# Kernel tuning notes

Measured on AMD Instinct MI355X. Metric: run time of the kernel, lower is better.

Reference implementation:

```python
import jax, jax.numpy as jnp
import numpy as np

B, T, C, V = 8, 2048, 256, 1024


def setup_inputs() -> dict:
    key = jax.random.key(0)
    k1, k2 = jax.random.split(key)
    z = jax.random.normal(k1, (B, T, C), dtype=jnp.float32)
    codebook = jax.random.normal(k2, (V, C), dtype=jnp.float32)
    mask = jnp.ones((B, T, 1), dtype=jnp.float32)
    return {"z": z, "codebook": codebook, "mask": mask}


def reference(z, codebook, mask):
    # e = codebook.embedding.weight.clone().detach()
    e = jax.lax.stop_gradient(codebook)            # (V, C)
    b, t, c = z.shape
    v = e.shape[0]
    zf = z.reshape(-1, c)                          # (B*T, C)
    # squared distances: ||z||^2 + ||e||^2 - 2 z e^T
    d = (jnp.sum(zf * zf, axis=1, keepdims=True)
         + jnp.sum(e * e, axis=1)
         - 2.0 * zf @ e.T)                         # (B*T, V)
    idx = jnp.argmin(d, axis=1)                    # (B*T,)
    # one-hot scatter + matmul gather == direct gather
    z_q = e[idx].reshape(b, t, c)
    z_q = z_q * mask
    pad_e = e[0]                                   # (C,)
    z_q = jnp.where(mask == 0, pad_e, z_q)
    # masked MSE commitment loss
    valid_count = jnp.sum(mask) * c
    commitment_loss = jnp.sum((z - jax.lax.stop_gradient(z_q)) ** 2 * mask) / valid_count
    # straight-through estimator
    z_q = z + jax.lax.stop_gradient(z_q - z)
    min_encoding_indices = idx.reshape(b, t)
    # run-length dedup (deterministic: keep first element of each run),
    # compacted to the front and padded with pad_e to static length T
    keep = jnp.concatenate(
        [jnp.ones((b, 1), bool),
         min_encoding_indices[:, 1:] != min_encoding_indices[:, :-1]], axis=1)
    order = jnp.argsort(jnp.where(keep, 0, 1), axis=1, stable=True)  # kept positions first
    gathered = jnp.take_along_axis(z_q, order[:, :, None], axis=1)
    kept_sorted = jnp.take_along_axis(keep, order, axis=1)
    z_q_disc = jnp.where(kept_sorted[:, :, None], gathered, pad_e)
    # softmax diversity loss over soft assignments
    soft = jax.nn.softmax(-d, axis=1)              # (B*T, V)
    hist = jnp.sum(soft * mask.reshape(-1, 1), axis=0)  # (V,)
    p = hist / (jnp.sum(hist) + 1e-8)
    diversity_loss = jnp.sum(p * jnp.log(p * v + 1e-8))
    return (commitment_loss, diversity_loss, z_q, z_q_disc, min_encoding_indices)
```

## Files before the change

kernel.cpp:

```cpp
#include <hip/hip_runtime.h>
#include <math.h>

#define NB 8
#define NT 2048
#define NC 256
#define NV 1024
#define BT (NB*NT)

typedef __attribute__((ext_vector_type(8)))  short bf16x8;
typedef __attribute__((ext_vector_type(8)))  short short8v;
typedef __attribute__((ext_vector_type(16))) float f32x16;

#define HIST_OFF  0
#define EN_OFF    4096
#define CPART_OFF 8192
#define ORD_OFF   16384
#define KC_OFF    77824
#define WS_REQ    77856

__device__ __forceinline__ float bf_hi(float v, short* bits) {
  unsigned u = __float_as_uint(v);
  *bits = (short)(u >> 16);
  return __uint_as_float(u & 0xffff0000u);
}

__global__ __launch_bounds__(256) void vq_prep_e(
    const float* __restrict__ e, short* __restrict__ e1,
    short* __restrict__ e2, short* __restrict__ e3)
{
  __shared__ float el[32 * NC];
  const int t = threadIdx.x, cb = blockIdx.x;
  {
    const int r = t >> 3, cc = (t & 7) * 32;
    const float* er = e + (size_t)(cb * 32 + r) * NC + cc;
    float* dst = el + r * NC + cc;
    #pragma unroll
    for (int i = 0; i < 8; ++i) *(float4*)(dst + i * 4) = *(const float4*)(er + i * 4);
  }
  __syncthreads();
  const int s = t >> 4, h = (t >> 3) & 1, rb = (t & 7) * 4;
  const int kb = s * 16 + h * 8;
  #pragma unroll
  for (int rr = 0; rr < 4; ++rr) {
    short8v p1, p2, p3;
    #pragma unroll
    for (int ii = 0; ii < 8; ++ii) {
      float v = el[(rb + rr) * NC + kb + ii];
      short b1, b2, b3;
      float f1 = bf_hi(v, &b1);
      float r1 = v - f1;
      float f2 = bf_hi(r1, &b2);
      float r2 = r1 - f2;
      bf_hi(r2, &b3);
      p1[ii] = b1; p2[ii] = b2; p3[ii] = b3;
    }
    size_t off = (size_t)(s * 2 + h) * 8192 + (size_t)(cb * 32 + rb + rr) * 8;
    *(short8v*)(e1 + off) = p1;
    *(short8v*)(e2 + off) = p2;
    *(short8v*)(e3 + off) = p3;
  }
}

__global__ void vq_enorm(const float* __restrict__ e, float* __restrict__ en) {
  int c = blockIdx.x, t = threadIdx.x;
  float v = e[(size_t)c * NC + t];
  float s = v * v;
  #pragma unroll
  for (int off = 32; off; off >>= 1) s += __shfl_down(s, off, 64);
  __shared__ float w4[4];
  if ((t & 63) == 0) w4[t >> 6] = s;
  __syncthreads();
  if (t == 0) en[c] = w4[0] + w4[1] + w4[2] + w4[3];
}

__global__ __launch_bounds__(512, 4) void vq_main_fused(
    const float* __restrict__ z,
    const short* __restrict__ eT1, const short* __restrict__ eT2, const short* __restrict__ eT3,
    const float* __restrict__ en, const float* __restrict__ mask,
    float* __restrict__ hist, float* __restrict__ idxf)
{
  __shared__ short zl1[8192], zl2[8192], zl3[8192];
  __shared__ float pmv[32][8];
  __shared__ int   pmi[32][8];
  __shared__ float psum[32][8];
  __shared__ float mfin[32];
  __shared__ float wrow[32];

  const int tid  = threadIdx.x;
  const int lane = tid & 63, wv = tid >> 6;
  const int l31  = lane & 31, half = lane >> 5;
  const int b = blockIdx.x, row0 = b * 32;

  {
    const int s = tid >> 5, r = tid & 31;
    const float* zp = z + (size_t)(row0 + r) * NC + s * 16;
    float v[16];
    #pragma unroll
    for (int i = 0; i < 4; ++i) *(float4*)(v + i * 4) = *(const float4*)(zp + i * 4);
    #pragma unroll
    for (int hh = 0; hh < 2; ++hh) {
      short8v p1, p2, p3;
      #pragma unroll
      for (int ii = 0; ii < 8; ++ii) {
        float x = v[hh * 8 + ii];
        short b1, b2, b3;
        float f1 = bf_hi(x, &b1);
        float r1 = x - f1;
        float f2 = bf_hi(r1, &b2);
        float r2 = r1 - f2;
        bf_hi(r2, &b3);
        p1[ii] = b1; p2[ii] = b2; p3[ii] = b3;
      }
      const int off = s * 512 + hh * 256 + r * 8;
      *(short8v*)&zl1[off] = p1;
      *(short8v*)&zl2[off] = p2;
      *(short8v*)&zl3[off] = p3;
    }
  }
  __syncthreads();

  f32x16 acc[4];
  #pragma unroll
  for (int t = 0; t < 4; ++t)
    #pragma unroll
    for (int r = 0; r < 16; ++r) acc[t][r] = 0.f;

  for (int s = 0; s < 16; ++s) {
    const int aoff = s * 512 + half * 256 + l31 * 8;
    const bf16x8 a1 = *(const bf16x8*)&zl1[aoff];
    const bf16x8 a2 = *(const bf16x8*)&zl2[aoff];
    const bf16x8 a3 = *(const bf16x8*)&zl3[aoff];
    const size_t bbase = (size_t)(s * 2 + half) * 8192 + (size_t)(wv * 128 + l31) * 8;
    #pragma unroll
    for (int t = 0; t < 4; ++t) {
      const size_t bo = bbase + (size_t)(t * 32) * 8;
      const bf16x8 b1 = *(const bf16x8*)(eT1 + bo);
      const bf16x8 b2 = *(const bf16x8*)(eT2 + bo);
      const bf16x8 b3 = *(const bf16x8*)(eT3 + bo);
      acc[t] = __builtin_amdgcn_mfma_f32_32x32x16_bf16(a1, b1, acc[t], 0, 0, 0);
      acc[t] = __builtin_amdgcn_mfma_f32_32x32x16_bf16(a2, b1, acc[t], 0, 0, 0);
      acc[t] = __builtin_amdgcn_mfma_f32_32x32x16_bf16(a3, b1, acc[t], 0, 0, 0);
      acc[t] = __builtin_amdgcn_mfma_f32_32x32x16_bf16(a1, b2, acc[t], 0, 0, 0);
      acc[t] = __builtin_amdgcn_mfma_f32_32x32x16_bf16(a2, b2, acc[t], 0, 0, 0);
      acc[t] = __builtin_amdgcn_mfma_f32_32x32x16_bf16(a1, b3, acc[t], 0, 0, 0);
    }
  }

  float enr[4];
  #pragma unroll
  for (int t = 0; t < 4; ++t) enr[t] = en[wv * 128 + t * 32 + l31];
  #pragma unroll
  for (int t = 0; t < 4; ++t)
    #pragma unroll
    for (int r = 0; r < 16; ++r) acc[t][r] = fmaf(-2.f, acc[t][r], enr[t]);

  float bv[16]; int bi[16];
  #pragma unroll
  for (int r = 0; r < 16; ++r) {
    bv[r] = acc[0][r]; bi[r] = wv * 128 + l31;
    #pragma unroll
    for (int t = 1; t < 4; ++t) {
      float vv = acc[t][r]; int cc = wv * 128 + t * 32 + l31;
      if (vv < bv[r]) { bv[r] = vv; bi[r] = cc; }
    }
    #pragma unroll
    for (int off = 1; off <= 16; off <<= 1) {
      float ov = __shfl_xor(bv[r], off, 64);
      int   oi = __shfl_xor(bi[r], off, 64);
      if (ov < bv[r] || (ov == bv[r] && oi < bi[r])) { bv[r] = ov; bi[r] = oi; }
    }
  }
  if (l31 == 0) {
    #pragma unroll
    for (int r = 0; r < 16; ++r) {
      int row = (r & 3) + 8 * (r >> 2) + 4 * half;
      pmv[row][wv] = bv[r]; pmi[row][wv] = bi[r];
    }
  }
  __syncthreads();
  if (tid < 32) {
    float mv = pmv[tid][0]; int mi = pmi[tid][0];
    #pragma unroll
    for (int w = 1; w < 8; ++w) {
      float v = pmv[tid][w]; int i2 = pmi[tid][w];
      if (v < mv || (v == mv && i2 < mi)) { mv = v; mi = i2; }
    }
    mfin[tid] = mv;
    idxf[row0 + tid] = (float)mi;
  }
  __syncthreads();

  #pragma unroll
  for (int r = 0; r < 16; ++r) {
    float m = mfin[(r & 3) + 8 * (r >> 2) + 4 * half];
    float s0 = 0.f;
    #pragma unroll
    for (int t = 0; t < 4; ++t) {
      float p = __expf(m - acc[t][r]);
      acc[t][r] = p; s0 += p;
    }
    #pragma unroll
    for (int off = 1; off <= 16; off <<= 1) s0 += __shfl_xor(s0, off, 64);
    if (l31 == 0) psum[(r & 3) + 8 * (r >> 2) + 4 * half][wv] = s0;
  }
  __syncthreads();
  if (tid < 32) {
    float s0 = 0.f;
    #pragma unroll
    for (int w = 0; w < 8; ++w) s0 += psum[tid][w];
    wrow[tid] = mask[row0 + tid] / s0;
  }
  __syncthreads();

  #pragma unroll
  for (int t = 0; t < 4; ++t) {
    float h = 0.f;
    #pragma unroll
    for (int r = 0; r < 16; ++r)
      h = fmaf(wrow[(r & 3) + 8 * (r >> 2) + 4 * half], acc[t][r], h);
    h += __shfl_xor(h, 32, 64);
    if (half == 0 && h > 1e-12f) atomicAdd(&hist[wv * 128 + t * 32 + l31], h);
  }
}

__global__ __launch_bounds__(256) void vq_gather(
    const float* __restrict__ z, const float* __restrict__ e,
    const float* __restrict__ mask, const float* __restrict__ idxf,
    float* __restrict__ zq, float* __restrict__ cpart)
{
  const int tid = threadIdx.x, bid = blockIdx.x;
  float cacc = 0.f;
  #pragma unroll
  for (int it = 0; it < 4; ++it) {
    int id  = bid * 1024 + it * 256 + tid;
    int row = id >> 6;
    int c4  = (id & 63) << 2;
    int idx = (int)idxf[row];
    float mv = mask[row];
    float4 zv = *(const float4*)(z + (size_t)row * NC + c4);
    float4 qv;
    if (mv == 0.0f) {
      qv = *(const float4*)(e + c4);
    } else {
      float4 ev = *(const float4*)(e + (size_t)idx * NC + c4);
      qv = make_float4(ev.x * mv, ev.y * mv, ev.z * mv, ev.w * mv);
    }
    *(float4*)(zq + (size_t)row * NC + c4) = qv;
    float dx = zv.x - qv.x, dy = zv.y - qv.y, dz = zv.z - qv.z, dw = zv.w - qv.w;
    cacc += (dx * dx + dy * dy + dz * dz + dw * dw) * mv;
  }
  #pragma unroll
  for (int off = 32; off; off >>= 1) cacc += __shfl_down(cacc, off, 64);
  __shared__ float w4[4];
  if ((tid & 63) == 0) w4[tid >> 6] = cacc;
  __syncthreads();
  if (tid == 0) cpart[bid] = w4[0] + w4[1] + w4[2] + w4[3];
}

__global__ void vq_scan(const float* __restrict__ idxf, int* __restrict__ ord, int* __restrict__ Kc) {
  int b = blockIdx.x, t = threadIdx.x;
  const float* ix = idxf + b * NT;
  int flags[8]; int cnt = 0; int base = t * 8;
  #pragma unroll
  for (int i = 0; i < 8; ++i) {
    int g = base + i;
    int k = (g == 0) ? 1 : (ix[g] != ix[g - 1] ? 1 : 0);
    flags[i] = k; cnt += k;
  }
  int lane = t & 63, wv = t >> 6;
  int scan = cnt;
  for (int off = 1; off < 64; off <<= 1) {
    int v = __shfl_up(scan, off, 64);
    if (lane >= off) scan += v;
  }
  __shared__ int wsum[4];
  if (lane == 63) wsum[wv] = scan;
  __syncthreads();
  int woff = 0;
  for (int w = 0; w < wv; ++w) woff += wsum[w];
  int pos = woff + scan - cnt;
  #pragma unroll
  for (int i = 0; i < 8; ++i) {
    if (flags[i]) { ord[b * NT + pos] = base + i; ++pos; }
  }
  if (t == 255) Kc[b] = woff + scan;
}

__global__ __launch_bounds__(256) void vq_disc(
    const float* __restrict__ zq, const float* __restrict__ e,
    const int* __restrict__ ord, const int* __restrict__ Kc,
    float* __restrict__ disc)
{
  const int tid = threadIdx.x, bid = blockIdx.x;
  #pragma unroll
  for (int it = 0; it < 2; ++it) {
    int id  = bid * 512 + it * 256 + tid;
    int row = id >> 6;
    int c4  = (id & 63) << 2;
    int b   = row >> 11;
    int j   = row & (NT - 1);
    int K   = Kc[b];
    float4 v;
    if (j < K) {
      int src = ord[(b << 11) + j];
      v = *(const float4*)(zq + ((size_t)(b << 11) + src) * NC + c4);
    } else {
      v = *(const float4*)(e + c4);
    }
    *(float4*)(disc + (size_t)row * NC + c4) = v;
  }
}

__global__ void vq_final(const float* __restrict__ hist, const float* __restrict__ cpart,
                         const float* __restrict__ mask, float* __restrict__ out) {
  int t = threadIdx.x;
  double csum = 0, msum = 0, hsum = 0;
  #pragma unroll
  for (int i = 0; i < 4; ++i) csum += (double)cpart[i * 256 + t];
  for (int i = t; i < BT; i += 256) msum += (double)mask[i];
  double h[4];
  #pragma unroll
  for (int i = 0; i < 4; ++i) { h[i] = (double)hist[i * 256 + t]; hsum += h[i]; }
  #pragma unroll
  for (int off = 32; off; off >>= 1) {
    csum += __shfl_down(csum, off, 64);
    msum += __shfl_down(msum, off, 64);
    hsum += __shfl_down(hsum, off, 64);
  }
  __shared__ double wc[4], wm[4], wh[4];
  __shared__ double tots[3];
  if ((t & 63) == 0) { int w = t >> 6; wc[w] = csum; wm[w] = msum; wh[w] = hsum; }
  __syncthreads();
  if (t == 0) {
    tots[0] = wc[0] + wc[1] + wc[2] + wc[3];
    tots[1] = wm[0] + wm[1] + wm[2] + wm[3];
    tots[2] = wh[0] + wh[1] + wh[2] + wh[3];
  }
  __syncthreads();
  double tot = tots[2] + 1e-8;
  double dv = 0;
  #pragma unroll
  for (int i = 0; i < 4; ++i) {
    double p = h[i] / tot;
    dv += p * log(p * 1024.0 + 1e-8);
  }
  #pragma unroll
  for (int off = 32; off; off >>= 1) dv += __shfl_down(dv, off, 64);
  if ((t & 63) == 0) wc[t >> 6] = dv;
  __syncthreads();
  if (t == 0) {
    out[1] = (float)(wc[0] + wc[1] + wc[2] + wc[3]);
    out[0] = (float)(tots[0] / (tots[1] * 256.0));
  }
}

extern "C" void kernel_launch(void* const* d_in, const int* in_sizes, int n_in,
                              void* d_out, int out_size, void* d_ws, size_t ws_size,
                              hipStream_t stream) {
  if (ws_size < (size_t)WS_REQ) return;

  const float* z    = (const float*)d_in[0];
  const float* e    = (const float*)d_in[1];
  const float* mask = (const float*)d_in[2];
  float* out = (float*)d_out;
  char* ws = (char*)d_ws;

  float* hist  = (float*)(ws + HIST_OFF);
  float* en    = (float*)(ws + EN_OFF);
  float* cpart = (float*)(ws + CPART_OFF);
  int*   ord   = (int*)(ws + ORD_OFF);
  int*   Kc    = (int*)(ws + KC_OFF);

  float* zq   = out + 2;
  float* disc = out + 2 + (size_t)BT * NC;
  float* idxf = out + 2 + (size_t)2 * BT * NC;

  short* e1 = (short*)disc;
  short* e2 = e1 + (size_t)NV * NC;
  short* e3 = e2 + (size_t)NV * NC;

  hipMemsetAsync(ws + HIST_OFF, 0, 4096, stream);
  vq_prep_e    <<<32, 256, 0, stream>>>(e, e1, e2, e3);
  vq_enorm     <<<NV, NC, 0, stream>>>(e, en);
  vq_main_fused<<<512, 512, 0, stream>>>(z, e1, e2, e3, en, mask, hist, idxf);
  vq_gather    <<<1024, 256, 0, stream>>>(z, e, mask, idxf, zq, cpart);
  vq_scan      <<<NB, 256, 0, stream>>>(idxf, ord, Kc);
  vq_disc      <<<2048, 256, 0, stream>>>(zq, e, ord, Kc, disc);
  vq_final     <<<1, NC, 0, stream>>>(hist, cpart, mask, out);
}
```

Before: 177.6 us.

## Process 64 rows per block in main kernel and fold mask sum into gather

The fused distance kernel now runs 1024-thread blocks covering 64 rows, with two M-tiles of waves sharing each codebook slice. This halves the number of times the bf16-split codebook is streamed from global memory per row. The mask sum is now reduced per block inside the gather kernel instead of in a serial 16K-element loop in the final single-block kernel, and the order buffer shrinks to 16-bit indices. The trade-offs are launch bounds of (1024,1), which may limit occupancy and register headroom, and only 256 blocks in the main kernel.

```diff
diff --git a/kernel.cpp b/kernel.cpp
--- a/kernel.cpp
+++ b/kernel.cpp
@@ -14,9 +14,10 @@
 #define HIST_OFF  0
 #define EN_OFF    4096
 #define CPART_OFF 8192
+#define MPART_OFF 12288
 #define ORD_OFF   16384
-#define KC_OFF    77824
-#define WS_REQ    77856
+#define KC_OFF    49152
+#define WS_REQ    49184
 
 __device__ __forceinline__ float bf_hi(float v, short* bits) {
   unsigned u = __float_as_uint(v);
@@ -73,26 +74,27 @@
   if (t == 0) en[c] = w4[0] + w4[1] + w4[2] + w4[3];
 }
 
-__global__ __launch_bounds__(512, 4) void vq_main_fused(
+__global__ __launch_bounds__(1024, 1) void vq_main_fused(
     const float* __restrict__ z,
     const short* __restrict__ eT1, const short* __restrict__ eT2, const short* __restrict__ eT3,
     const float* __restrict__ en, const float* __restrict__ mask,
     float* __restrict__ hist, float* __restrict__ idxf)
 {
-  __shared__ short zl1[8192], zl2[8192], zl3[8192];
-  __shared__ float pmv[32][8];
-  __shared__ int   pmi[32][8];
-  __shared__ float psum[32][8];
-  __shared__ float mfin[32];
-  __shared__ float wrow[32];
+  __shared__ short zl1[16384], zl2[16384], zl3[16384];
+  __shared__ float pmv[64][8];
+  __shared__ int   pmi[64][8];
+  __shared__ float psum[64][8];
+  __shared__ float mfin[64];
+  __shared__ float wrow[64];
 
   const int tid  = threadIdx.x;
   const int lane = tid & 63, wv = tid >> 6;
   const int l31  = lane & 31, half = lane >> 5;
-  const int b = blockIdx.x, row0 = b * 32;
+  const int mt   = wv >> 3, nq = wv & 7;
+  const int b = blockIdx.x, row0 = b * 64;
 
   {
-    const int s = tid >> 5, r = tid & 31;
+    const int s = wv, r = lane;
     const float* zp = z + (size_t)(row0 + r) * NC + s * 16;
     float v[16];
     #pragma unroll
@@ -111,7 +113,7 @@
         bf_hi(r2, &b3);
         p1[ii] = b1; p2[ii] = b2; p3[ii] = b3;
       }
-      const int off = s * 512 + hh * 256 + r * 8;
+      const int off = (s * 2 + hh) * 512 + r * 8;
       *(short8v*)&zl1[off] = p1;
       *(short8v*)&zl2[off] = p2;
       *(short8v*)&zl3[off] = p3;
@@ -126,11 +128,11 @@
     for (int r = 0; r < 16; ++r) acc[t][r] = 0.f;
 
   for (int s = 0; s < 16; ++s) {
-    const int aoff = s * 512 + half * 256 + l31 * 8;
+    const int aoff = (s * 2 + half) * 512 + (mt * 32 + l31) * 8;
     const bf16x8 a1 = *(const bf16x8*)&zl1[aoff];
     const bf16x8 a2 = *(const bf16x8*)&zl2[aoff];
     const bf16x8 a3 = *(const bf16x8*)&zl3[aoff];
-    const size_t bbase = (size_t)(s * 2 + half) * 8192 + (size_t)(wv * 128 + l31) * 8;
+    const size_t bbase = (size_t)(s * 2 + half) * 8192 + (size_t)(nq * 128 + l31) * 8;
     #pragma unroll
     for (int t = 0; t < 4; ++t) {
       const size_t bo = bbase + (size_t)(t * 32) * 8;
@@ -148,7 +150,7 @@
 
   float enr[4];
   #pragma unroll
-  for (int t = 0; t < 4; ++t) enr[t] = en[wv * 128 + t * 32 + l31];
+  for (int t = 0; t < 4; ++t) enr[t] = en[nq * 128 + t * 32 + l31];
   #pragma unroll
   for (int t = 0; t < 4; ++t)
     #pragma unroll
@@ -157,10 +159,10 @@
   float bv[16]; int bi[16];
   #pragma unroll
   for (int r = 0; r < 16; ++r) {
-    bv[r] = acc[0][r]; bi[r] = wv * 128 + l31;
+    bv[r] = acc[0][r]; bi[r] = nq * 128 + l31;
     #pragma unroll
     for (int t = 1; t < 4; ++t) {
-      float vv = acc[t][r]; int cc = wv * 128 + t * 32 + l31;
+      float vv = acc[t][r]; int cc = nq * 128 + t * 32 + l31;
       if (vv < bv[r]) { bv[r] = vv; bi[r] = cc; }
     }
     #pragma unroll
@@ -173,12 +175,12 @@
   if (l31 == 0) {
     #pragma unroll
     for (int r = 0; r < 16; ++r) {
-      int row = (r & 3) + 8 * (r >> 2) + 4 * half;
-      pmv[row][wv] = bv[r]; pmi[row][wv] = bi[r];
-    }
-  }
-  __syncthreads();
-  if (tid < 32) {
+      int rowb = mt * 32 + (r & 3) + 8 * (r >> 2) + 4 * half;
+      pmv[rowb][nq] = bv[r]; pmi[rowb][nq] = bi[r];
+    }
+  }
+  __syncthreads();
+  if (tid < 64) {
     float mv = pmv[tid][0]; int mi = pmi[tid][0];
     #pragma unroll
     for (int w = 1; w < 8; ++w) {
@@ -192,7 +194,8 @@
 
   #pragma unroll
   for (int r = 0; r < 16; ++r) {
-    float m = mfin[(r & 3) + 8 * (r >> 2) + 4 * half];
+    const int rowb = mt * 32 + (r & 3) + 8 * (r >> 2) + 4 * half;
+    float m = mfin[rowb];
     float s0 = 0.f;
     #pragma unroll
     for (int t = 0; t < 4; ++t) {
@@ -201,10 +204,10 @@
     }
     #pragma unroll
     for (int off = 1; off <= 16; off <<= 1) s0 += __shfl_xor(s0, off, 64);
-    if (l31 == 0) psum[(r & 3) + 8 * (r >> 2) + 4 * half][wv] = s0;
-  }
-  __syncthreads();
-  if (tid < 32) {
+    if (l31 == 0) psum[rowb][nq] = s0;
+  }
+  __syncthreads();
+  if (tid < 64) {
     float s0 = 0.f;
     #pragma unroll
     for (int w = 0; w < 8; ++w) s0 += psum[tid][w];
@@ -217,19 +220,19 @@
     float h = 0.f;
     #pragma unroll
     for (int r = 0; r < 16; ++r)
-      h = fmaf(wrow[(r & 3) + 8 * (r >> 2) + 4 * half], acc[t][r], h);
+      h = fmaf(wrow[mt * 32 + (r & 3) + 8 * (r >> 2) + 4 * half], acc[t][r], h);
     h += __shfl_xor(h, 32, 64);
-    if (half == 0 && h > 1e-12f) atomicAdd(&hist[wv * 128 + t * 32 + l31], h);
+    if (half == 0 && h > 1e-12f) atomicAdd(&hist[nq * 128 + t * 32 + l31], h);
   }
 }
 
 __global__ __launch_bounds__(256) void vq_gather(
     const float* __restrict__ z, const float* __restrict__ e,
     const float* __restrict__ mask, const float* __restrict__ idxf,
-    float* __restrict__ zq, float* __restrict__ cpart)
+    float* __restrict__ zq, float* __restrict__ cpart, float* __restrict__ mpart)
 {
   const int tid = threadIdx.x, bid = blockIdx.x;
-  float cacc = 0.f;
+  float cacc = 0.f, macc = 0.f;
   #pragma unroll
   for (int it = 0; it < 4; ++it) {
     int id  = bid * 1024 + it * 256 + tid;
@@ -248,16 +251,24 @@
     *(float4*)(zq + (size_t)row * NC + c4) = qv;
     float dx = zv.x - qv.x, dy = zv.y - qv.y, dz = zv.z - qv.z, dw = zv.w - qv.w;
     cacc += (dx * dx + dy * dy + dz * dz + dw * dw) * mv;
-  }
-  #pragma unroll
-  for (int off = 32; off; off >>= 1) cacc += __shfl_down(cacc, off, 64);
-  __shared__ float w4[4];
-  if ((tid & 63) == 0) w4[tid >> 6] = cacc;
-  __syncthreads();
-  if (tid == 0) cpart[bid] = w4[0] + w4[1] + w4[2] + w4[3];
-}
-
-__global__ void vq_scan(const float* __restrict__ idxf, int* __restrict__ ord, int* __restrict__ Kc) {
+    macc += mv;
+  }
+  #pragma unroll
+  for (int off = 32; off; off >>= 1) {
+    cacc += __shfl_down(cacc, off, 64);
+    macc += __shfl_down(macc, off, 64);
+  }
+  __shared__ float w4[4], m4[4];
+  if ((tid & 63) == 0) { w4[tid >> 6] = cacc; m4[tid >> 6] = macc; }
+  __syncthreads();
+  if (tid == 0) {
+    cpart[bid] = w4[0] + w4[1] + w4[2] + w4[3];
+    mpart[bid] = (m4[0] + m4[1] + m4[2] + m4[3]) * (1.0f / 64.0f);
+  }
+}
+
+__global__ void vq_scan(const float* __restrict__ idxf, unsigned short* __restrict__ ord,
+                        int* __restrict__ Kc) {
   int b = blockIdx.x, t = threadIdx.x;
   const float* ix = idxf + b * NT;
   int flags[8]; int cnt = 0; int base = t * 8;
@@ -281,14 +292,14 @@
   int pos = woff + scan - cnt;
   #pragma unroll
   for (int i = 0; i < 8; ++i) {
-    if (flags[i]) { ord[b * NT + pos] = base + i; ++pos; }
+    if (flags[i]) { ord[b * NT + pos] = (unsigned short)(base + i); ++pos; }
   }
   if (t == 255) Kc[b] = woff + scan;
 }
 
 __global__ __launch_bounds__(256) void vq_disc(
     const float* __restrict__ zq, const float* __restrict__ e,
-    const int* __restrict__ ord, const int* __restrict__ Kc,
+    const unsigned short* __restrict__ ord, const int* __restrict__ Kc,
     float* __restrict__ disc)
 {
   const int tid = threadIdx.x, bid = blockIdx.x;
@@ -312,12 +323,14 @@
 }
 
 __global__ void vq_final(const float* __restrict__ hist, const float* __restrict__ cpart,
-                         const float* __restrict__ mask, float* __restrict__ out) {
+                         const float* __restrict__ mpart, float* __restrict__ out) {
   int t = threadIdx.x;
   double csum = 0, msum = 0, hsum = 0;
   #pragma unroll
-  for (int i = 0; i < 4; ++i) csum += (double)cpart[i * 256 + t];
-  for (int i = t; i < BT; i += 256) msum += (double)mask[i];
+  for (int i = 0; i < 4; ++i) {
+    csum += (double)cpart[i * 256 + t];
+    msum += (double)mpart[i * 256 + t];
+  }
   double h[4];
   #pragma unroll
   for (int i = 0; i < 4; ++i) { h[i] = (double)hist[i * 256 + t]; hsum += h[i]; }
@@ -365,11 +378,12 @@
   float* out = (float*)d_out;
   char* ws = (char*)d_ws;
 
-  float* hist  = (float*)(ws + HIST_OFF);
-  float* en    = (float*)(ws + EN_OFF);
-  float* cpart = (float*)(ws + CPART_OFF);
-  int*   ord   = (int*)(ws + ORD_OFF);
-  int*   Kc    = (int*)(ws + KC_OFF);
+  float*          hist  = (float*)(ws + HIST_OFF);
+  float*          en    = (float*)(ws + EN_OFF);
+  float*          cpart = (float*)(ws + CPART_OFF);
+  float*          mpart = (float*)(ws + MPART_OFF);
+  unsigned short* ord   = (unsigned short*)(ws + ORD_OFF);
+  int*            Kc    = (int*)(ws + KC_OFF);
 
   float* zq   = out + 2;
   float* disc = out + 2 + (size_t)BT * NC;
@@ -382,9 +396,9 @@
   hipMemsetAsync(ws + HIST_OFF, 0, 4096, stream);
   vq_prep_e    <<<32, 256, 0, stream>>>(e, e1, e2, e3);
   vq_enorm     <<<NV, NC, 0, stream>>>(e, en);
-  vq_main_fused<<<512, 512, 0, stream>>>(z, e1, e2, e3, en, mask, hist, idxf);
-  vq_gather    <<<1024, 256, 0, stream>>>(z, e, mask, idxf, zq, cpart);
+  vq_main_fused<<<256, 1024, 0, stream>>>(z, e1, e2, e3, en, mask, hist, idxf);
+  vq_gather    <<<1024, 256, 0, stream>>>(z, e, mask, idxf, zq, cpart, mpart);
   vq_scan      <<<NB, 256, 0, stream>>>(idxf, ord, Kc);
   vq_disc      <<<2048, 256, 0, stream>>>(zq, e, ord, Kc, disc);
-  vq_final     <<<1, NC, 0, stream>>>(hist, cpart, mask, out);
-}
+  vq_final     <<<1, NC, 0, stream>>>(hist, cpart, mpart, out);
+}
```

After: 169.0 us. -4.8%, faster.
